# Optimization experiments

Measured on AMD Instinct MI355X. Metric: run time of the kernel, lower is better.

The kernel has to match this reference:

```python
import jax, jax.numpy as jnp
import numpy as np

T, B, IN, OUT, N_MOD, K = 1024, 8, 1024, 1024, 16, 2

def setup_inputs() -> dict:
    key = jax.random.key(0)
    k1, k2, k3, k4 = jax.random.split(key, 4)
    x = jax.random.normal(k1, (T, B, IN), dtype=jnp.float32)
    selection = jax.random.randint(k2, (B, K), 0, N_MOD, dtype=jnp.int64)
    weight = jax.random.normal(k3, (N_MOD, IN, OUT), dtype=jnp.float32) * (1.0 / np.sqrt(IN))
    bias = jax.random.normal(k4, (N_MOD, OUT), dtype=jnp.float32) * 0.02
    return {"x": x, "selection": selection, "weight": weight, "bias": bias}

def reference(x, selection, weight, bias):
    # time_major=True: x is [T, B, in] -> batch-major [B, T, in]
    xb = jnp.swapaxes(x, 0, 1)
    # Gather the K selected expert weight matrices per batch row: [B, K, in, out]
    W_sel = weight[selection]
    # Equivalent to matmul(x[i], cat(weight[sel], dim=1)): [B, T, K, out]
    o = jnp.einsum('bti,bkio->btko', xb, W_sel)
    Bn, Tn, Kn, On = o.shape
    o = o.reshape(Bn, Tn, Kn * On)
    # concat_dim == 1 bias: bias[sel].view(1, -1) -> [1, K*out], broadcast over T
    o = o + bias[selection].reshape(Bn, 1, Kn * On)
    # back to time-major [T, B, K*out]
    return jnp.swapaxes(o, 0, 1)
```

## Files before the change

### kernel.cpp

```cpp
#include <hip/hip_runtime.h>

#define T_DIM 1024
#define B_DIM 8
#define IN_DIM 1024
#define OUT_DIM 1024
#define N_MODL 16
#define K_SEL 2

typedef unsigned short ushort_t;
typedef __bf16 bf16x8 __attribute__((ext_vector_type(8)));
typedef float f32x4 __attribute__((ext_vector_type(4)));

__device__ __forceinline__ unsigned int f2bf2(float lo, float hi) {
  union { float f; unsigned int u; } a, b; a.f = lo; b.f = hi;
  unsigned int ra = (a.u + 0x7fffu + ((a.u >> 16) & 1u)) >> 16;
  unsigned int rb = (b.u + 0x7fffu + ((b.u >> 16) & 1u)) >> 16;
  return ra | (rb << 16);
}
__device__ __forceinline__ unsigned short f2bf(float f) {
  union { float f; unsigned int u; } v; v.f = f;
  return (unsigned short)((v.u + 0x7fffu + ((v.u >> 16) & 1u)) >> 16);
}

__device__ __forceinline__ void async_g2l(const void* g, void* l) {
  __builtin_amdgcn_global_load_lds(
      (const __attribute__((address_space(1))) unsigned int*)g,
      (__attribute__((address_space(3))) unsigned int*)l,
      16, 0, 0);
}

__global__ __launch_bounds__(256) void convert_x_kernel(const float* __restrict__ x,
                                                        ushort_t* __restrict__ xb) {
  const int i = blockIdx.x * 256 + threadIdx.x;
  const float4* s = (const float4*)x;
  float4 a = s[i * 2], b = s[i * 2 + 1];
  uint4 o;
  o.x = f2bf2(a.x, a.y); o.y = f2bf2(a.z, a.w);
  o.z = f2bf2(b.x, b.y); o.w = f2bf2(b.z, b.w);
  ((uint4*)xb)[i] = o;
}

__global__ __launch_bounds__(256) void convert_w_kernel(const float* __restrict__ w,
                                                        ushort_t* __restrict__ wt) {
  __shared__ float tile[64][65];
  const int m = blockIdx.z;
  const int i0 = blockIdx.x * 64;
  const int o0 = blockIdx.y * 64;
  const float* src = w + ((size_t)m * IN_DIM + i0) * OUT_DIM + o0;
  const int c = (threadIdx.x & 15) * 4;
  const int r0 = threadIdx.x >> 4;
#pragma unroll
  for (int p = 0; p < 4; ++p) {
    const int r = r0 + p * 16;
    float4 v = *(const float4*)(src + (size_t)r * OUT_DIM + c);
    tile[r][c + 0] = v.x; tile[r][c + 1] = v.y;
    tile[r][c + 2] = v.z; tile[r][c + 3] = v.w;
  }
  __syncthreads();
  ushort_t* dst = wt + ((size_t)m * OUT_DIM + o0) * IN_DIM + i0;
#pragma unroll
  for (int p = 0; p < 4; ++p) {
    const int r = r0 + p * 16;
    ushort4 ov;
    ov.x = f2bf(tile[c + 0][r]);
    ov.y = f2bf(tile[c + 1][r]);
    ov.z = f2bf(tile[c + 2][r]);
    ov.w = f2bf(tile[c + 3][r]);
    *(ushort4*)(dst + (size_t)r * IN_DIM + c) = ov;
  }
}

__device__ __forceinline__ int read_sel(const int* __restrict__ s, int g) {
  bool i64 = true;
#pragma unroll
  for (int j = 0; j < 8; ++j) i64 &= (s[2 * j + 1] == 0);
  return i64 ? s[2 * g] : s[g];
}

__global__ __launch_bounds__(256, 4) void mlgemm_kernel(const ushort_t* __restrict__ xb,
                                                        const ushort_t* __restrict__ wt,
                                                        const int* __restrict__ selp,
                                                        const float* __restrict__ bias,
                                                        float* __restrict__ out) {
  __shared__ ushort_t As[128 * 64];
  __shared__ ushort_t Bs[128 * 64];

  const int g = blockIdx.z;
  const int b = g >> 1, ks = g & 1;
  const int e = read_sel(selp, g);

  const ushort_t* A  = xb + (size_t)b * IN_DIM;
  const ushort_t* Bm = wt + (size_t)e * OUT_DIM * IN_DIM;
  const float* bp = bias + (size_t)e * OUT_DIM;

  const int m0 = blockIdx.y * 128;
  const int n0 = blockIdx.x * 128;

  const int tid = threadIdx.x;
  const int lane = tid & 63;
  const int wv = tid >> 6;

  const int srow = lane >> 3;
  const int sx = (((lane & 7) ^ (srow & 7)) << 3);
  const ushort_t* Ab = A  + (size_t)(m0 + srow) * (B_DIM * IN_DIM) + sx;
  const ushort_t* Bb = Bm + (size_t)(n0 + srow) * IN_DIM + sx;

  const int frow = lane & 15;
  const int quad = lane >> 4;
  const int cbase = ((quad ^ (frow & 7)) << 3);
  const int wrow = (wv & 1) * 64;
  const int wcol = (wv >> 1) * 64;
  const ushort_t* Ard = As + (wrow + frow) * 64;
  const ushort_t* Brd = Bs + (wcol + frow) * 64;

  f32x4 acc[4][4] = {};

  for (int k0 = 0; k0 < IN_DIM; k0 += 64) {
#pragma unroll
    for (int c = 0; c < 4; ++c) {
      const int j = wv * 4 + c;
      async_g2l(Ab + (size_t)(8 * j) * (B_DIM * IN_DIM) + k0, As + j * 512);
      async_g2l(Bb + (size_t)(8 * j) * IN_DIM + k0, Bs + j * 512);
    }
    __syncthreads();
#pragma unroll
    for (int kk = 0; kk < 64; kk += 32) {
      const int coff = cbase ^ kk;
      bf16x8 af[4], bfr[4];
#pragma unroll
      for (int i = 0; i < 4; ++i) {
        af[i]  = *(const bf16x8*)(Ard + i * 16 * 64 + coff);
        bfr[i] = *(const bf16x8*)(Brd + i * 16 * 64 + coff);
      }
#pragma unroll
      for (int mt = 0; mt < 4; ++mt)
#pragma unroll
        for (int nt = 0; nt < 4; ++nt)
          acc[mt][nt] = __builtin_amdgcn_mfma_f32_16x16x32_bf16(af[mt], bfr[nt],
                                                                acc[mt][nt], 0, 0, 0);
    }
    __syncthreads();
  }

  const int orow0 = m0 + wrow + (quad * 4);
  const int ocol0 = n0 + wcol + frow;
  float bv[4];
#pragma unroll
  for (int nt = 0; nt < 4; ++nt) bv[nt] = bp[ocol0 + nt * 16];
  float* Cb = out + (size_t)b * (K_SEL * OUT_DIM) + (size_t)ks * OUT_DIM;
#pragma unroll
  for (int mt = 0; mt < 4; ++mt) {
#pragma unroll
    for (int r = 0; r < 4; ++r) {
      const size_t rowoff = (size_t)(orow0 + mt * 16 + r) * (B_DIM * K_SEL * OUT_DIM);
#pragma unroll
      for (int nt = 0; nt < 4; ++nt)
        Cb[rowoff + ocol0 + nt * 16] = acc[mt][nt][r] + bv[nt];
    }
  }
}

extern "C" void kernel_launch(void* const* d_in, const int* in_sizes, int n_in,
                              void* d_out, int out_size, void* d_ws, size_t ws_size,
                              hipStream_t stream) {
  const float* x    = (const float*)d_in[0];
  const int*   sel  = (const int*)d_in[1];
  const float* w    = (const float*)d_in[2];
  const float* bias = (const float*)d_in[3];
  float* out = (float*)d_out;

  ushort_t* xb = (ushort_t*)d_ws;
  ushort_t* wt = (ushort_t*)((char*)d_ws +
                             (size_t)T_DIM * B_DIM * IN_DIM * 2);

  convert_x_kernel<<<dim3(T_DIM * B_DIM * IN_DIM / 8 / 256), 256, 0, stream>>>(x, xb);
  convert_w_kernel<<<dim3(IN_DIM / 64, OUT_DIM / 64, N_MODL), 256, 0, stream>>>(w, wt);
  mlgemm_kernel<<<dim3(OUT_DIM / 128, T_DIM / 128, B_DIM * K_SEL), 256, 0, stream>>>(
      xb, wt, sel, bias, out);
}
```

Measured before the change: 186.9 us.

## Share A tile across both selected experts and merge conversion kernels

Each GEMM block now computes both selected experts for a batch row, loading the x tile into LDS once and reusing it against two weight tiles, with two accumulator sets. This halves the x reads and the grid size and doubles the MFMA work per block. The x and weight conversion kernels are fused into one launch to save a kernel launch. In exchange, register pressure doubles (launch bounds drop to 2 blocks per CU) and the grid falls to 512 blocks, which may cut occupancy and latency hiding.

```diff
diff --git a/kernel.cpp b/kernel.cpp
--- a/kernel.cpp
+++ b/kernel.cpp
@@ -29,23 +29,26 @@
       16, 0, 0);
 }
 
-__global__ __launch_bounds__(256) void convert_x_kernel(const float* __restrict__ x,
-                                                        ushort_t* __restrict__ xb) {
-  const int i = blockIdx.x * 256 + threadIdx.x;
-  const float4* s = (const float4*)x;
-  float4 a = s[i * 2], b = s[i * 2 + 1];
-  uint4 o;
-  o.x = f2bf2(a.x, a.y); o.y = f2bf2(a.z, a.w);
-  o.z = f2bf2(b.x, b.y); o.w = f2bf2(b.z, b.w);
-  ((uint4*)xb)[i] = o;
-}
-
-__global__ __launch_bounds__(256) void convert_w_kernel(const float* __restrict__ w,
-                                                        ushort_t* __restrict__ wt) {
+__global__ __launch_bounds__(256) void convert_kernel(const float* __restrict__ x,
+                                                      const float* __restrict__ w,
+                                                      ushort_t* __restrict__ xb,
+                                                      ushort_t* __restrict__ wt) {
   __shared__ float tile[64][65];
-  const int m = blockIdx.z;
-  const int i0 = blockIdx.x * 64;
-  const int o0 = blockIdx.y * 64;
+  const int bid = blockIdx.x;
+  if (bid >= 4096) {
+    const int i = (bid - 4096) * 256 + threadIdx.x;
+    const float4* s = (const float4*)x;
+    float4 a = s[i * 2], b = s[i * 2 + 1];
+    uint4 o;
+    o.x = f2bf2(a.x, a.y); o.y = f2bf2(a.z, a.w);
+    o.z = f2bf2(b.x, b.y); o.w = f2bf2(b.z, b.w);
+    ((uint4*)xb)[i] = o;
+    return;
+  }
+  const int m = bid >> 8;
+  const int rest = bid & 255;
+  const int i0 = (rest & 15) * 64;
+  const int o0 = (rest >> 4) * 64;
   const float* src = w + ((size_t)m * IN_DIM + i0) * OUT_DIM + o0;
   const int c = (threadIdx.x & 15) * 4;
   const int r0 = threadIdx.x >> 4;
@@ -77,85 +80,100 @@
   return i64 ? s[2 * g] : s[g];
 }
 
-__global__ __launch_bounds__(256, 4) void mlgemm_kernel(const ushort_t* __restrict__ xb,
+__global__ __launch_bounds__(256, 2) void mlgemm_kernel(const ushort_t* __restrict__ xb,
                                                         const ushort_t* __restrict__ wt,
                                                         const int* __restrict__ selp,
                                                         const float* __restrict__ bias,
                                                         float* __restrict__ out) {
   __shared__ ushort_t As[128 * 64];
-  __shared__ ushort_t Bs[128 * 64];
+  __shared__ ushort_t Bs[2][128 * 64];
 
-  const int g = blockIdx.z;
-  const int b = g >> 1, ks = g & 1;
-  const int e = read_sel(selp, g);
+  const int b = blockIdx.z;
+  const int e0 = read_sel(selp, 2 * b);
+  const int e1 = read_sel(selp, 2 * b + 1);
 
   const ushort_t* A  = xb + (size_t)b * IN_DIM;
-  const ushort_t* Bm = wt + (size_t)e * OUT_DIM * IN_DIM;
-  const float* bp = bias + (size_t)e * OUT_DIM;
+  const ushort_t* B0 = wt + (size_t)e0 * OUT_DIM * IN_DIM;
+  const ushort_t* B1 = wt + (size_t)e1 * OUT_DIM * IN_DIM;
 
   const int m0 = blockIdx.y * 128;
   const int n0 = blockIdx.x * 128;
 
-  const int tid = threadIdx.x;
-  const int lane = tid & 63;
-  const int wv = tid >> 6;
+  const int lane = threadIdx.x & 63;
+  const int wv = threadIdx.x >> 6;
 
   const int srow = lane >> 3;
   const int sx = (((lane & 7) ^ (srow & 7)) << 3);
-  const ushort_t* Ab = A  + (size_t)(m0 + srow) * (B_DIM * IN_DIM) + sx;
-  const ushort_t* Bb = Bm + (size_t)(n0 + srow) * IN_DIM + sx;
+  const ushort_t* Ab  = A  + (size_t)(m0 + srow) * (B_DIM * IN_DIM) + sx;
+  const ushort_t* Bb0 = B0 + (size_t)(n0 + srow) * IN_DIM + sx;
+  const ushort_t* Bb1 = B1 + (size_t)(n0 + srow) * IN_DIM + sx;
 
   const int frow = lane & 15;
   const int quad = lane >> 4;
   const int cbase = ((quad ^ (frow & 7)) << 3);
   const int wrow = (wv & 1) * 64;
   const int wcol = (wv >> 1) * 64;
-  const ushort_t* Ard = As + (wrow + frow) * 64;
-  const ushort_t* Brd = Bs + (wcol + frow) * 64;
+  const ushort_t* Ard  = As    + (wrow + frow) * 64;
+  const ushort_t* Brd0 = Bs[0] + (wcol + frow) * 64;
+  const ushort_t* Brd1 = Bs[1] + (wcol + frow) * 64;
 
-  f32x4 acc[4][4] = {};
+  f32x4 acc0[4][4] = {};
+  f32x4 acc1[4][4] = {};
 
   for (int k0 = 0; k0 < IN_DIM; k0 += 64) {
 #pragma unroll
     for (int c = 0; c < 4; ++c) {
       const int j = wv * 4 + c;
-      async_g2l(Ab + (size_t)(8 * j) * (B_DIM * IN_DIM) + k0, As + j * 512);
-      async_g2l(Bb + (size_t)(8 * j) * IN_DIM + k0, Bs + j * 512);
+      async_g2l(Ab  + (size_t)(8 * j) * (B_DIM * IN_DIM) + k0, As + j * 512);
+      async_g2l(Bb0 + (size_t)(8 * j) * IN_DIM + k0, Bs[0] + j * 512);
+      async_g2l(Bb1 + (size_t)(8 * j) * IN_DIM + k0, Bs[1] + j * 512);
     }
     __syncthreads();
 #pragma unroll
     for (int kk = 0; kk < 64; kk += 32) {
       const int coff = cbase ^ kk;
-      bf16x8 af[4], bfr[4];
+      bf16x8 af[4], bf0[4], bf1[4];
 #pragma unroll
       for (int i = 0; i < 4; ++i) {
-        af[i]  = *(const bf16x8*)(Ard + i * 16 * 64 + coff);
-        bfr[i] = *(const bf16x8*)(Brd + i * 16 * 64 + coff);
+        af[i]  = *(const bf16x8*)(Ard  + i * 16 * 64 + coff);
+        bf0[i] = *(const bf16x8*)(Brd0 + i * 16 * 64 + coff);
+        bf1[i] = *(const bf16x8*)(Brd1 + i * 16 * 64 + coff);
       }
 #pragma unroll
       for (int mt = 0; mt < 4; ++mt)
 #pragma unroll
-        for (int nt = 0; nt < 4; ++nt)
-          acc[mt][nt] = __builtin_amdgcn_mfma_f32_16x16x32_bf16(af[mt], bfr[nt],
-                                                                acc[mt][nt], 0, 0, 0);
+        for (int nt = 0; nt < 4; ++nt) {
+          acc0[mt][nt] = __builtin_amdgcn_mfma_f32_16x16x32_bf16(af[mt], bf0[nt],
+                                                                 acc0[mt][nt], 0, 0, 0);
+          acc1[mt][nt] = __builtin_amdgcn_mfma_f32_16x16x32_bf16(af[mt], bf1[nt],
+                                                                 acc1[mt][nt], 0, 0, 0);
+        }
     }
     __syncthreads();
   }
 
-  const int orow0 = m0 + wrow + (quad * 4);
+  const int orow0 = m0 + wrow + quad * 4;
   const int ocol0 = n0 + wcol + frow;
-  float bv[4];
+  const float* bp0 = bias + (size_t)e0 * OUT_DIM;
+  const float* bp1 = bias + (size_t)e1 * OUT_DIM;
+  float bv0[4], bv1[4];
 #pragma unroll
-  for (int nt = 0; nt < 4; ++nt) bv[nt] = bp[ocol0 + nt * 16];
-  float* Cb = out + (size_t)b * (K_SEL * OUT_DIM) + (size_t)ks * OUT_DIM;
+  for (int nt = 0; nt < 4; ++nt) {
+    bv0[nt] = bp0[ocol0 + nt * 16];
+    bv1[nt] = bp1[ocol0 + nt * 16];
+  }
+  float* C0 = out + (size_t)b * (K_SEL * OUT_DIM);
+  float* C1 = C0 + OUT_DIM;
 #pragma unroll
   for (int mt = 0; mt < 4; ++mt) {
 #pragma unroll
     for (int r = 0; r < 4; ++r) {
       const size_t rowoff = (size_t)(orow0 + mt * 16 + r) * (B_DIM * K_SEL * OUT_DIM);
 #pragma unroll
-      for (int nt = 0; nt < 4; ++nt)
-        Cb[rowoff + ocol0 + nt * 16] = acc[mt][nt][r] + bv[nt];
+      for (int nt = 0; nt < 4; ++nt) {
+        C0[rowoff + ocol0 + nt * 16] = acc0[mt][nt][r] + bv0[nt];
+        C1[rowoff + ocol0 + nt * 16] = acc1[mt][nt][r] + bv1[nt];
+      }
     }
   }
 }
@@ -173,8 +191,8 @@
   ushort_t* wt = (ushort_t*)((char*)d_ws +
                              (size_t)T_DIM * B_DIM * IN_DIM * 2);
 
-  convert_x_kernel<<<dim3(T_DIM * B_DIM * IN_DIM / 8 / 256), 256, 0, stream>>>(x, xb);
-  convert_w_kernel<<<dim3(IN_DIM / 64, OUT_DIM / 64, N_MODL), 256, 0, stream>>>(w, wt);
-  mlgemm_kernel<<<dim3(OUT_DIM / 128, T_DIM / 128, B_DIM * K_SEL), 256, 0, stream>>>(
+  convert_kernel<<<dim3(4096 + T_DIM * B_DIM * IN_DIM / 8 / 256), 256, 0, stream>>>(
+      x, w, xb, wt);
+  mlgemm_kernel<<<dim3(OUT_DIM / 128, T_DIM / 128, B_DIM), 256, 0, stream>>>(
       xb, wt, sel, bias, out);
 }
```

After: 183.5 us. About the same (-1.8%).
